# Performance work log

Measured on AMD Instinct MI355X. Metric: run time of the kernel, lower is better.

## Reference

```python
import jax, jax.numpy as jnp
import numpy as np

KERNEL_MUL = 2.0
KERNEL_NUM = 5


def setup_inputs() -> dict:
    key = jax.random.key(0)
    k1, k2 = jax.random.split(key)
    source = jax.random.normal(k1, (4096, 256), dtype=jnp.float32)
    target = jax.random.normal(k2, (4096, 256), dtype=jnp.float32)
    return {"source": source, "target": target}


def _mmd(source, target):
    b = source.shape[0]
    total = jnp.concatenate([source, target], axis=0)  # [2N, D]
    n = total.shape[0]
    # pairwise squared L2 via gram trick (avoids O(N^2 * D) intermediate)
    sq = jnp.sum(total * total, axis=1)  # [2N]
    d2 = sq[:, None] + sq[None, :] - 2.0 * (total @ total.T)
    d2 = jnp.maximum(d2, 0.0)  # [2N, 2N]
    # bandwidth from detached distances (matches L2_distance.data)
    bandwidth = jax.lax.stop_gradient(jnp.sum(d2)) / (n * n - n)
    bandwidth = bandwidth / (KERNEL_MUL ** (KERNEL_NUM // 2))
    kernels = jnp.zeros_like(d2)
    for i in range(KERNEL_NUM):
        kernels = kernels + jnp.exp(-d2 / (bandwidth * KERNEL_MUL ** i))
    XX = kernels[:b, :b]
    YY = kernels[b:, b:]
    XY = kernels[:b, b:]
    YX = kernels[b:, :b]
    return jnp.mean(XX + YY - XY - YX)


def reference(source, target):
    return _mmd(source, target)
```

## Files before the change

### kernel.cpp

```cpp
#include <hip/hip_runtime.h>
#include <hip/hip_bf16.h>


#define N_TOTAL 8192
#define B_HALF 4096
#define D_DIM 256
#define TILE 128
#define NTILE 64
#define NTRI 2080

typedef float f32x16 __attribute__((ext_vector_type(16)));
typedef _Float16 f16x8 __attribute__((ext_vector_type(8)));

__device__ __forceinline__ const float* row_base(const float* src, const float* tgt, int r) {
    return (r < B_HALF) ? src + (size_t)r * D_DIM : tgt + (size_t)(r - B_HALF) * D_DIM;
}

__global__ __launch_bounds__(256) void prep_kernel(const float* __restrict__ src,
                                                   const float* __restrict__ tgt,
                                                   _Float16* __restrict__ a16f,
                                                   float* __restrict__ sq,
                                                   float* __restrict__ colpart) {
    int tid = threadIdx.x, w = tid >> 6, lane = tid & 63;
    int r0 = blockIdx.x * 32;

    #pragma unroll
    for (int i = 0; i < 8; ++i) {
        int row = r0 + w * 8 + i;
        const float* rp = row_base(src, tgt, row);
        float4 v = ((const float4*)rp)[lane];
        float s = v.x*v.x + v.y*v.y + v.z*v.z + v.w*v.w;
        #pragma unroll
        for (int off = 32; off; off >>= 1) s += __shfl_down(s, off, 64);
        if (lane == 0) sq[row] = s;
    }

    float c = 0.f;
    for (int r = r0; r < r0 + 32; ++r)
        c += row_base(src, tgt, r)[tid];
    colpart[blockIdx.x * D_DIM + tid] = c;

    int wg = blockIdx.x * 4 + w;
    #pragma unroll
    for (int i = 0; i < 4; ++i) {
        int t  = wg * 4 + i;
        int kb = t >> 7, rg = t & 127;
        int row = rg * 64 + lane;
        const float* rp = row_base(src, tgt, row) + kb * 8;
        float4 v0 = ((const float4*)rp)[0];
        float4 v1 = ((const float4*)rp)[1];
        _Float16 h[8] = {(_Float16)v0.x, (_Float16)v0.y, (_Float16)v0.z, (_Float16)v0.w,
                         (_Float16)v1.x, (_Float16)v1.y, (_Float16)v1.z, (_Float16)v1.w};
        *(f16x8*)(a16f + ((size_t)kb * N_TOTAL + row) * 8) = *(f16x8*)h;
    }
}

__global__ __launch_bounds__(256) void bw_kernel(const float* __restrict__ sq,
                                                 const float* __restrict__ colpart,
                                                 float* __restrict__ negc,
                                                 double* __restrict__ accum) {
    __shared__ double red[256];
    int t = threadIdx.x;
    double s = 0.0;
    for (int i = t; i < N_TOTAL; i += 256) s += (double)sq[i];
    red[t] = s;
    __syncthreads();
    for (int off = 128; off; off >>= 1) {
        if (t < off) red[t] += red[t + off];
        __syncthreads();
    }
    double sumsq = red[0];
    __syncthreads();
    float c = 0.f;
    for (int k = 0; k < 256; ++k) c += colpart[k * D_DIM + t];
    red[t] = (double)c * (double)c;
    __syncthreads();
    for (int off = 128; off; off >>= 1) {
        if (t < off) red[t] += red[t + off];
        __syncthreads();
    }
    if (t == 0) {
        double S1 = 2.0 * (double)N_TOTAL * sumsq - 2.0 * red[0];
        double nn = (double)N_TOTAL * (double)N_TOTAL - (double)N_TOTAL;
        double bw = S1 / nn / 4.0;
        negc[0] = (float)(-1.4426950408889634 / (16.0 * bw));
        accum[0] = 0.0;
    }
}

__global__ __launch_bounds__(256, 4) void mmd_main(const _Float16* __restrict__ a16f,
                                                   const float* __restrict__ sq,
                                                   const float* __restrict__ negc,
                                                   double* __restrict__ accum) {
    __shared__ float wsum[4];

    int b  = blockIdx.x;
    int bs = (b & 7) * (NTRI / 8) + (b >> 3);
    int it = 0, cum = 0;
    while (cum + (NTILE - it) <= bs) { cum += NTILE - it; ++it; }
    int jt = it + (bs - cum);

    int tid = threadIdx.x, lane = tid & 63, wid = tid >> 6;
    int wrow = wid >> 1, wcol = wid & 1;
    int rowA = it * TILE, rowB = jt * TILE;
    int c32 = lane & 31, khalf = lane >> 5;

    const _Float16* PA = a16f + (size_t)khalf * (N_TOTAL * 8)
                              + (size_t)(rowA + wrow * 64 + c32) * 8;
    const _Float16* PB = a16f + (size_t)khalf * (N_TOTAL * 8)
                              + (size_t)(rowB + wcol * 64 + c32) * 8;

    f32x16 acc[2][2] = {};

    #pragma unroll 4
    for (int kap = 0; kap < 16; ++kap) {
        size_t ko = (size_t)kap * (N_TOTAL * 16);
        f16x8 af[2], bf[2];
        af[0] = *(const f16x8*)(PA + ko);
        af[1] = *(const f16x8*)(PA + ko + 32 * 8);
        bf[0] = *(const f16x8*)(PB + ko);
        bf[1] = *(const f16x8*)(PB + ko + 32 * 8);
        __builtin_amdgcn_s_setprio(1);
        #pragma unroll
        for (int mt = 0; mt < 2; ++mt)
            #pragma unroll
            for (int nt = 0; nt < 2; ++nt)
                acc[mt][nt] = __builtin_amdgcn_mfma_f32_32x32x16_f16(af[mt], bf[nt], acc[mt][nt], 0, 0, 0);
        __builtin_amdgcn_s_setprio(0);
    }

    float nc = *negc;
    float sjn[2];
    #pragma unroll
    for (int nt = 0; nt < 2; ++nt)
        sjn[nt] = sq[rowB + wcol * 64 + nt * 32 + c32];
    float tsum = 0.f;
    #pragma unroll
    for (int mt = 0; mt < 2; ++mt) {
        #pragma unroll
        for (int reg = 0; reg < 16; ++reg) {
            int i = rowA + wrow * 64 + mt * 32 + (reg & 3) + 8 * (reg >> 2) + 4 * khalf;
            float si = sq[i];
            #pragma unroll
            for (int nt = 0; nt < 2; ++nt) {
                float d2 = fmaxf(si + sjn[nt] - 2.0f * acc[mt][nt][reg], 0.f);
                float u  = exp2f(nc * d2);
                float u2 = u * u, u4 = u2 * u2, u8 = u4 * u4;
                tsum += u + u2 + u4 + u8 + u8 * u8;
            }
        }
    }
    float scale = (((it < 32) == (jt < 32)) ? 1.f : -1.f) * ((it == jt) ? 1.f : 2.f);
    tsum *= scale;

    #pragma unroll
    for (int off = 32; off; off >>= 1) tsum += __shfl_down(tsum, off, 64);
    if (lane == 0) wsum[wid] = tsum;
    __syncthreads();
    if (tid == 0) {
        float t = wsum[0] + wsum[1] + wsum[2] + wsum[3];
        atomicAdd(accum, (double)t);
    }
}

__global__ void finalize_kernel(const double* __restrict__ accum, float* __restrict__ out) {
    out[0] = (float)(accum[0] / ((double)B_HALF * (double)B_HALF));
}

extern "C" void kernel_launch(void* const* d_in, const int* in_sizes, int n_in,
                              void* d_out, int out_size, void* d_ws, size_t ws_size,
                              hipStream_t stream) {
    const float* src = (const float*)d_in[0];
    const float* tgt = (const float*)d_in[1];
    float* out = (float*)d_out;

    char* ws = (char*)d_ws;
    float*  sq      = (float*)ws;
    float*  colpart = (float*)(ws + 32768);
    float*  negc    = (float*)(ws + 294912);
    double* accum   = (double*)(ws + 294920);
    _Float16* a16f  = (_Float16*)(ws + 327680);

    prep_kernel<<<256, 256, 0, stream>>>(src, tgt, a16f, sq, colpart);
    bw_kernel<<<1, 256, 0, stream>>>(sq, colpart, negc, accum);
    mmd_main<<<NTRI, 256, 0, stream>>>(a16f, sq, negc, accum);
    finalize_kernel<<<1, 1, 0, stream>>>(accum, out);
}
```

Before: 71.87 us.

## Use 512-thread blocks covering tile pairs, fold finalize into main kernel

The main kernel now launches 512-thread blocks, each covering a row tile against two adjacent column tiles. This cuts the block count from 2080 to 1056 and shares A-tile loads across more waves. Below-diagonal waves get zero scale, so some MFMA and exp work is wasted. The epilogue pre-scales the squared norms by the exponent constant and uses FMA chains to trim VALU work. The finalize launch is replaced by a last-block counter with threadfence, which removes one kernel launch.

```diff
diff --git a/kernel.cpp b/kernel.cpp
--- a/kernel.cpp
+++ b/kernel.cpp
@@ -5,9 +5,8 @@
 #define N_TOTAL 8192
 #define B_HALF 4096
 #define D_DIM 256
-#define TILE 128
 #define NTILE 64
-#define NTRI 2080
+#define NPAIR 1056
 
 typedef float f32x16 __attribute__((ext_vector_type(16)));
 typedef _Float16 f16x8 __attribute__((ext_vector_type(8)));
@@ -20,9 +19,11 @@
                                                    const float* __restrict__ tgt,
                                                    _Float16* __restrict__ a16f,
                                                    float* __restrict__ sq,
-                                                   float* __restrict__ colpart) {
+                                                   float* __restrict__ colpart,
+                                                   unsigned* __restrict__ cnt) {
     int tid = threadIdx.x, w = tid >> 6, lane = tid & 63;
     int r0 = blockIdx.x * 32;
+    if (blockIdx.x == 0 && tid == 0) *cnt = 0;
 
     #pragma unroll
     for (int i = 0; i < 8; ++i) {
@@ -88,27 +89,31 @@
     }
 }
 
-__global__ __launch_bounds__(256, 4) void mmd_main(const _Float16* __restrict__ a16f,
-                                                   const float* __restrict__ sq,
-                                                   const float* __restrict__ negc,
-                                                   double* __restrict__ accum) {
-    __shared__ float wsum[4];
+__global__ __launch_bounds__(512) void mmd_main(const _Float16* __restrict__ a16f,
+                                                const float* __restrict__ sq,
+                                                const float* __restrict__ negc,
+                                                double* __restrict__ accum,
+                                                unsigned* __restrict__ cnt,
+                                                float* __restrict__ out) {
+    __shared__ float wsum[8];
 
     int b  = blockIdx.x;
-    int bs = (b & 7) * (NTRI / 8) + (b >> 3);
+    int bs = (b & 7) * (NPAIR / 8) + (b >> 3);
     int it = 0, cum = 0;
-    while (cum + (NTILE - it) <= bs) { cum += NTILE - it; ++it; }
-    int jt = it + (bs - cum);
+    while (cum + (32 - (it >> 1)) <= bs) { cum += 32 - (it >> 1); ++it; }
+    int p = (it >> 1) + (bs - cum);
 
     int tid = threadIdx.x, lane = tid & 63, wid = tid >> 6;
-    int wrow = wid >> 1, wcol = wid & 1;
-    int rowA = it * TILE, rowB = jt * TILE;
+    int wrow = wid >> 2, wcol = wid & 3;
+    int jt   = 2 * p + (wcol >> 1);
+    int rowA = it * 128 + wrow * 64;
+    int rowB = jt * 128 + (wcol & 1) * 64;
     int c32 = lane & 31, khalf = lane >> 5;
 
     const _Float16* PA = a16f + (size_t)khalf * (N_TOTAL * 8)
-                              + (size_t)(rowA + wrow * 64 + c32) * 8;
+                              + (size_t)(rowA + c32) * 8;
     const _Float16* PB = a16f + (size_t)khalf * (N_TOTAL * 8)
-                              + (size_t)(rowB + wcol * 64 + c32) * 8;
+                              + (size_t)(rowB + c32) * 8;
 
     f32x16 acc[2][2] = {};
 
@@ -130,41 +135,51 @@
     }
 
     float nc = *negc;
-    float sjn[2];
+    float m2nc = -2.f * nc;
+    float sj1[2];
     #pragma unroll
     for (int nt = 0; nt < 2; ++nt)
-        sjn[nt] = sq[rowB + wcol * 64 + nt * 32 + c32];
-    float tsum = 0.f;
+        sj1[nt] = nc * sq[rowB + nt * 32 + c32];
+    float tu = 0.f, t2 = 0.f;
     #pragma unroll
     for (int mt = 0; mt < 2; ++mt) {
         #pragma unroll
         for (int reg = 0; reg < 16; ++reg) {
-            int i = rowA + wrow * 64 + mt * 32 + (reg & 3) + 8 * (reg >> 2) + 4 * khalf;
-            float si = sq[i];
+            int i = rowA + mt * 32 + (reg & 3) + 8 * (reg >> 2) + 4 * khalf;
+            float si1 = nc * sq[i];
             #pragma unroll
             for (int nt = 0; nt < 2; ++nt) {
-                float d2 = fmaxf(si + sjn[nt] - 2.0f * acc[mt][nt][reg], 0.f);
-                float u  = exp2f(nc * d2);
+                float e  = fminf(fmaf(m2nc, acc[mt][nt][reg], si1 + sj1[nt]), 0.f);
+                float u  = exp2f(e);
                 float u2 = u * u, u4 = u2 * u2, u8 = u4 * u4;
-                tsum += u + u2 + u4 + u8 + u8 * u8;
+                float in2 = fmaf(u4, 1.f + u8, 1.f);
+                float in3 = fmaf(u2, in2, 1.f);
+                tu += u;
+                t2  = fmaf(u2, in3, t2);
             }
         }
     }
-    float scale = (((it < 32) == (jt < 32)) ? 1.f : -1.f) * ((it == jt) ? 1.f : 2.f);
-    tsum *= scale;
+    float scale = 0.f;
+    if (jt >= it)
+        scale = (((it < 32) == (jt < 32)) ? 1.f : -1.f) * ((it == jt) ? 1.f : 2.f);
+    float tsum = (tu + t2) * scale;
 
     #pragma unroll
     for (int off = 32; off; off >>= 1) tsum += __shfl_down(tsum, off, 64);
     if (lane == 0) wsum[wid] = tsum;
     __syncthreads();
     if (tid == 0) {
-        float t = wsum[0] + wsum[1] + wsum[2] + wsum[3];
+        float t = 0.f;
+        #pragma unroll
+        for (int w = 0; w < 8; ++w) t += wsum[w];
         atomicAdd(accum, (double)t);
-    }
-}
-
-__global__ void finalize_kernel(const double* __restrict__ accum, float* __restrict__ out) {
-    out[0] = (float)(accum[0] / ((double)B_HALF * (double)B_HALF));
+        __threadfence();
+        unsigned old = atomicAdd(cnt, 1u);
+        if (old == NPAIR - 1) {
+            double v = atomicAdd(accum, 0.0);
+            out[0] = (float)(v / ((double)B_HALF * (double)B_HALF));
+        }
+    }
 }
 
 extern "C" void kernel_launch(void* const* d_in, const int* in_sizes, int n_in,
@@ -175,14 +190,14 @@
     float* out = (float*)d_out;
 
     char* ws = (char*)d_ws;
-    float*  sq      = (float*)ws;
-    float*  colpart = (float*)(ws + 32768);
-    float*  negc    = (float*)(ws + 294912);
-    double* accum   = (double*)(ws + 294920);
-    _Float16* a16f  = (_Float16*)(ws + 327680);
-
-    prep_kernel<<<256, 256, 0, stream>>>(src, tgt, a16f, sq, colpart);
+    float*    sq      = (float*)ws;
+    float*    colpart = (float*)(ws + 32768);
+    float*    negc    = (float*)(ws + 294912);
+    double*   accum   = (double*)(ws + 294920);
+    unsigned* cnt     = (unsigned*)(ws + 294928);
+    _Float16* a16f    = (_Float16*)(ws + 327680);
+
+    prep_kernel<<<256, 256, 0, stream>>>(src, tgt, a16f, sq, colpart, cnt);
     bw_kernel<<<1, 256, 0, stream>>>(sq, colpart, negc, accum);
-    mmd_main<<<NTRI, 256, 0, stream>>>(a16f, sq, negc, accum);
-    finalize_kernel<<<1, 1, 0, stream>>>(accum, out);
-}
+    mmd_main<<<NPAIR, 512, 0, stream>>>(a16f, sq, negc, accum, cnt, out);
+}
```

Result: slower. 86.11 us (+19.8%).
